# Kernel optimization log

Hardware: AMD Instinct MI355X
Metric: run time of the kernel (lower is better)

Reference implementation:

```python
import jax, jax.numpy as jnp
import numpy as np

DIM = 1024
MULT = 4
HID = DIM * MULT
E = 8
B, S = 2, 2048


def _rmsnorm(x):
    # zeta SimpleRMSNorm: F.normalize(x, dim=-1) * sqrt(dim)
    n = jnp.linalg.norm(x, axis=-1, keepdims=True)
    return x / jnp.maximum(n, 1e-12) * jnp.sqrt(jnp.asarray(x.shape[-1], x.dtype))


def _act_quant(x):
    # per-token 8-bit absmax quant (BitNet b1.58), straight-through in fwd math
    scale = 127.0 / jnp.clip(jnp.max(jnp.abs(x), axis=-1, keepdims=True), 1e-5)
    q = jnp.clip(jnp.round(x * scale), -128, 127) / scale
    return x + jax.lax.stop_gradient(q - x)


def _w_quant(w, axes):
    # ternary weight quant with per-matrix mean-abs scale
    scale = 1.0 / jnp.clip(jnp.mean(jnp.abs(w), axis=axes, keepdims=True), 1e-5)
    q = jnp.clip(jnp.round(w * scale), -1, 1) / scale
    return w + jax.lax.stop_gradient(q - w)


def setup_inputs() -> dict:
    key = jax.random.key(0)
    ks = jax.random.split(key, 8)
    sd = 0.02
    x = jax.random.normal(ks[0], (B, S, DIM), dtype=jnp.float32)
    gw = jax.random.normal(ks[1], (E, DIM), dtype=jnp.float32) * sd
    gb = jnp.zeros((E,), dtype=jnp.float32)
    w1 = jax.random.normal(ks[2], (E, HID, DIM), dtype=jnp.float32) * sd
    b1 = jnp.zeros((E, HID), dtype=jnp.float32)
    w2 = jax.random.normal(ks[3], (E, DIM, HID), dtype=jnp.float32) * sd
    b2 = jnp.zeros((E, DIM), dtype=jnp.float32)
    return {"x": x, "gw": gw, "gb": gb, "w1": w1, "b1": b1, "w2": w2, "b2": b2}


def reference(x, gw, gb, w1, b1, w2, b2):
    # BitLinear input preprocessing: RMSNorm then 8-bit activation quant
    xq = _act_quant(_rmsnorm(x))  # [B,S,D]

    # Gate: softmax(BitLinear(dim, E))
    logits = jnp.einsum("bsd,ed->bse", xq, _w_quant(gw, axes=(0, 1))) + gb
    gates = jax.nn.softmax(logits, axis=-1)  # [B,S,E]

    # Experts: BitLinear -> GELU -> BitLinear, quant scales per expert
    w1q = _w_quant(w1, axes=(1, 2))  # [E,H,D]
    w2q = _w_quant(w2, axes=(1, 2))  # [E,D,H]
    h = jnp.einsum("bsd,ehd->bseh", xq, w1q) + b1  # [B,S,E,H]
    a = jax.nn.gelu(h, approximate=False)
    aq = _act_quant(_rmsnorm(a))
    expert_out = jnp.einsum("bseh,edh->bsed", aq, w2q) + b2  # [B,S,E,D]

    # softmax-weighted sum over experts
    return jnp.einsum("bse,bsed->bsd", gates, expert_out)
```

## Files before the change

### kernel.cpp

```cpp
#include <hip/hip_runtime.h>


#define T_TOK 4096
#define DIMS  1024
#define HID   4096
#define NE    8
#define ROWB  8192ull

typedef __attribute__((ext_vector_type(4))) int       i32x4;
typedef __attribute__((ext_vector_type(8))) _Float16  f16x8;

__device__ __forceinline__ float block_sum(float v, float* buf, int tid) {
  #pragma unroll
  for (int o = 32; o > 0; o >>= 1) v += __shfl_down(v, o, 64);
  __syncthreads();
  if ((tid & 63) == 0) buf[tid >> 6] = v;
  __syncthreads();
  return buf[0] + buf[1] + buf[2] + buf[3];
}
__device__ __forceinline__ float block_max(float v, float* buf, int tid) {
  #pragma unroll
  for (int o = 32; o > 0; o >>= 1) { float t = __shfl_down(v, o, 64); v = fmaxf(v, t); }
  __syncthreads();
  if ((tid & 63) == 0) buf[tid >> 6] = v;
  __syncthreads();
  return fmaxf(fmaxf(buf[0], buf[1]), fmaxf(buf[2], buf[3]));
}

__device__ __forceinline__ void gl_lds16(const void* g, void* l) {
  __builtin_amdgcn_global_load_lds(
      (const __attribute__((address_space(1))) unsigned int*)g,
      (__attribute__((address_space(3))) unsigned int*)l, 16, 0, 0);
}

__device__ __forceinline__ int q8(float v) {
  return ((int)fminf(fmaxf(rintf(v), -128.0f), 127.0f)) & 0xff;
}

__device__ __forceinline__ const i32x4* frag(const char* s, int row, int ckW) {
  return (const i32x4*)&s[row * 128 + ((ckW ^ (row & 7)) << 4)];
}

__global__ __launch_bounds__(256) void wabs_sum_kernel(
    const float4* __restrict__ w, int n_f4, int shift, float* __restrict__ sums) {
  __shared__ float buf[4];
  const int tid = threadIdx.x;
  const int base = blockIdx.x * 4096;
  float acc = 0.0f;
  for (int k = 0; k < 16; ++k) {
    int fi = base + k * 256 + tid;
    if (fi < n_f4) {
      float4 v = w[fi];
      acc += fabsf(v.x) + fabsf(v.y) + fabsf(v.z) + fabsf(v.w);
    }
  }
  acc = block_sum(acc, buf, tid);
  if (tid == 0) atomicAdd(&sums[base >> shift], acc);
}

__global__ void mkscales_kernel(const float* __restrict__ wsum, float* __restrict__ sc) {
  if (threadIdx.x == 0) {
    #pragma unroll
    for (int e = 0; e < NE; ++e) {
      float m1 = fmaxf(wsum[e] * (1.0f / 4194304.0f), 1e-5f);
      sc[e] = m1; sc[8 + e] = 1.0f / m1;
      float m2 = fmaxf(wsum[8 + e] * (1.0f / 4194304.0f), 1e-5f);
      sc[16 + e] = m2; sc[24 + e] = 1.0f / m2;
    }
    float mg = fmaxf(wsum[16] * (1.0f / 8192.0f), 1e-5f);
    sc[32] = mg; sc[33] = 1.0f / mg;
  }
}

__global__ __launch_bounds__(256) void wquant_kernel(
    const float4* __restrict__ w, int* __restrict__ o, int n_f4, int shift,
    const float* __restrict__ qs) {
  int fi = blockIdx.x * 256 + threadIdx.x;
  if (fi >= n_f4) return;
  const float s = qs[fi >> shift];
  float4 v = w[fi];
  int b0 = ((int)fminf(fmaxf(rintf(v.x * s), -1.0f), 1.0f)) & 0xff;
  int b1 = ((int)fminf(fmaxf(rintf(v.y * s), -1.0f), 1.0f)) & 0xff;
  int b2 = ((int)fminf(fmaxf(rintf(v.z * s), -1.0f), 1.0f)) & 0xff;
  int b3 = ((int)fminf(fmaxf(rintf(v.w * s), -1.0f), 1.0f)) & 0xff;
  o[fi] = b0 | (b1 << 8) | (b2 << 16) | (b3 << 24);
}

__global__ __launch_bounds__(256) void preprocess_kernel(
    const float* __restrict__ x, const float* __restrict__ gw,
    const float* __restrict__ gb, const float* __restrict__ scales,
    int* __restrict__ qx, float* __restrict__ inv_sx, float* __restrict__ gates) {
  __shared__ float buf[4];
  const int t = blockIdx.x, tid = threadIdx.x;
  const float4 xv = ((const float4*)(x + (size_t)t * DIMS))[tid];
  float ss = xv.x * xv.x + xv.y * xv.y + xv.z * xv.z + xv.w * xv.w;
  ss = block_sum(ss, buf, tid);
  const float rr = 32.0f / fmaxf(sqrtf(ss), 1e-12f);
  const float y0 = xv.x * rr, y1 = xv.y * rr, y2 = xv.z * rr, y3 = xv.w * rr;
  float am = fmaxf(fmaxf(fabsf(y0), fabsf(y1)), fmaxf(fabsf(y2), fabsf(y3)));
  am = block_max(am, buf, tid);
  const float aclip = fmaxf(am, 1e-5f);
  const float qsc = 127.0f / aclip;
  const float q0 = fminf(fmaxf(rintf(y0 * qsc), -128.0f), 127.0f);
  const float q1 = fminf(fmaxf(rintf(y1 * qsc), -128.0f), 127.0f);
  const float q2 = fminf(fmaxf(rintf(y2 * qsc), -128.0f), 127.0f);
  const float q3 = fminf(fmaxf(rintf(y3 * qsc), -128.0f), 127.0f);
  qx[t * 256 + tid] = (((int)q0) & 0xff) | ((((int)q1) & 0xff) << 8) |
                      ((((int)q2) & 0xff) << 16) | ((((int)q3) & 0xff) << 24);

  const float gsabs = scales[32], gqs = scales[33];
  float lg[NE];
  #pragma unroll
  for (int e = 0; e < NE; ++e) {
    const float4 gv = ((const float4*)(gw + e * DIMS))[tid];
    float t0 = fminf(fmaxf(rintf(gv.x * gqs), -1.0f), 1.0f);
    float t1 = fminf(fmaxf(rintf(gv.y * gqs), -1.0f), 1.0f);
    float t2 = fminf(fmaxf(rintf(gv.z * gqs), -1.0f), 1.0f);
    float t3 = fminf(fmaxf(rintf(gv.w * gqs), -1.0f), 1.0f);
    lg[e] = q0 * t0 + q1 * t1 + q2 * t2 + q3 * t3;
  }
  #pragma unroll
  for (int e = 0; e < NE; ++e) lg[e] = block_sum(lg[e], buf, tid);
  if (tid == 0) {
    const float isx = aclip / 127.0f;
    inv_sx[t] = isx;
    float l[NE], mx = -1e30f;
    #pragma unroll
    for (int e = 0; e < NE; ++e) { l[e] = lg[e] * (isx * gsabs) + gb[e]; mx = fmaxf(mx, l[e]); }
    float s = 0.0f;
    #pragma unroll
    for (int e = 0; e < NE; ++e) { l[e] = expf(l[e] - mx); s += l[e]; }
    const float inv = 1.0f / s;
    #pragma unroll
    for (int e = 0; e < NE; ++e) gates[t * NE + e] = l[e] * inv;
  }
}

__global__ __launch_bounds__(256, 2) void gemm1_kernel(
    const char* __restrict__ qx, const char* __restrict__ w1q,
    const float* __restrict__ scales, const float* __restrict__ inv_sx,
    const float* __restrict__ b1, char* __restrict__ aqa) {
  __shared__ __align__(16) char sA[256 * 128];
  __shared__ __align__(16) char sB[128 * 128];
  const int e = blockIdx.z;
  const char* A = qx;
  const char* Bm = w1q + (size_t)e * HID * DIMS;
  char* obase = aqa + (size_t)e * T_TOK * ROWB;
  const int n0 = blockIdx.x * 128, m0 = blockIdx.y * 256;
  const int tid = threadIdx.x, lane = tid & 63, wv = tid >> 6;
  const int wr = (wv >> 1) * 128, wc = (wv & 1) * 64, lm = lane & 15, lq = lane >> 4;
  i32x4 acc[8][4] = {};
  for (int k0 = 0; k0 < DIMS; k0 += 128) {
    #pragma unroll
    for (int it = 0; it < 8; ++it) {
      const int c = it * 256 + tid;
      const int row = c >> 3, ckG = (c & 7) ^ (row & 7);
      gl_lds16(A + (size_t)(m0 + row) * DIMS + k0 + ckG * 16, &sA[c * 16]);
    }
    #pragma unroll
    for (int it = 0; it < 4; ++it) {
      const int c = it * 256 + tid;
      const int row = c >> 3, ckG = (c & 7) ^ (row & 7);
      gl_lds16(Bm + (size_t)(n0 + row) * DIMS + k0 + ckG * 16, &sB[c * 16]);
    }
    __syncthreads();
    #pragma unroll
    for (int kk = 0; kk < 2; ++kk) {
      i32x4 av[8], bv[4];
      const int ckW = kk * 4 + lq;
      #pragma unroll
      for (int i = 0; i < 8; ++i) av[i] = *frag(sA, wr + i * 16 + lm, ckW);
      #pragma unroll
      for (int j = 0; j < 4; ++j) bv[j] = *frag(sB, wc + j * 16 + lm, ckW);
      #pragma unroll
      for (int i = 0; i < 8; ++i)
        #pragma unroll
        for (int j = 0; j < 4; ++j)
          acc[i][j] = __builtin_amdgcn_mfma_i32_16x16x64_i8(av[i], bv[j], acc[i][j], 0, 0, 0);
    }
    __syncthreads();
  }
  const float s1 = scales[e];
  #pragma unroll
  for (int i = 0; i < 8; ++i) {
    #pragma unroll
    for (int r = 0; r < 4; ++r) {
      const int row = m0 + wr + i * 16 + lq * 4 + r;
      const float rs = inv_sx[row] * s1;
      _Float16* orow = (_Float16*)(obase + (size_t)row * ROWB);
      #pragma unroll
      for (int j = 0; j < 4; ++j) {
        const int col = n0 + wc + j * 16 + lm;
        const float h = (float)acc[i][j][r] * rs + b1[e * HID + col];
        const float a = 0.5f * h * (1.0f + erff(h * 0.70710678118654752f));
        orow[col] = (_Float16)a;
      }
    }
  }
}

__global__ __launch_bounds__(256) void rowquant_kernel(
    char* __restrict__ aqa, float* __restrict__ inv_sa) {
  __shared__ float buf[4];
  const size_t R = blockIdx.x;
  char* rowb = aqa + R * ROWB;
  const int tid = threadIdx.x;
  f16x8 v0 = ((const f16x8*)rowb)[tid * 2];
  f16x8 v1 = ((const f16x8*)rowb)[tid * 2 + 1];
  float f[16];
  #pragma unroll
  for (int k = 0; k < 8; ++k) { f[k] = (float)v0[k]; f[8 + k] = (float)v1[k]; }
  float ss = 0.0f;
  #pragma unroll
  for (int k = 0; k < 16; ++k) ss += f[k] * f[k];
  ss = block_sum(ss, buf, tid);
  const float rr = 64.0f / fmaxf(sqrtf(ss), 1e-12f);
  float am = 0.0f;
  #pragma unroll
  for (int k = 0; k < 16; ++k) am = fmaxf(am, fabsf(f[k] * rr));
  am = block_max(am, buf, tid);
  const float aclip = fmaxf(am, 1e-5f);
  const float qsc = rr * 127.0f / aclip;
  int4 o;
  o.x = q8(f[0] * qsc) | (q8(f[1] * qsc) << 8) | (q8(f[2] * qsc) << 16) | (q8(f[3] * qsc) << 24);
  o.y = q8(f[4] * qsc) | (q8(f[5] * qsc) << 8) | (q8(f[6] * qsc) << 16) | (q8(f[7] * qsc) << 24);
  o.z = q8(f[8] * qsc) | (q8(f[9] * qsc) << 8) | (q8(f[10] * qsc) << 16) | (q8(f[11] * qsc) << 24);
  o.w = q8(f[12] * qsc) | (q8(f[13] * qsc) << 8) | (q8(f[14] * qsc) << 16) | (q8(f[15] * qsc) << 24);
  ((int4*)rowb)[tid] = o;
  if (tid == 0) inv_sa[R] = aclip / 127.0f;
}

__global__ __launch_bounds__(256, 2) void gemm2_kernel(
    const char* __restrict__ aqa, const char* __restrict__ w2q,
    const float* __restrict__ scales, const float* __restrict__ inv_sa,
    const float* __restrict__ b2, const float* __restrict__ gates,
    float* __restrict__ dst, int use_atomic) {
  __shared__ __align__(16) char sA[256 * 128];
  __shared__ __align__(16) char sB[128 * 128];
  const int e = blockIdx.z;
  const char* A = aqa + (size_t)e * T_TOK * ROWB;
  const char* Bm = w2q + (size_t)e * DIMS * HID;
  const int n0 = blockIdx.x * 128, m0 = blockIdx.y * 256;
  const int tid = threadIdx.x, lane = tid & 63, wv = tid >> 6;
  const int wr = (wv >> 1) * 128, wc = (wv & 1) * 64, lm = lane & 15, lq = lane >> 4;
  i32x4 acc[8][4] = {};
  for (int k0 = 0; k0 < HID; k0 += 128) {
    #pragma unroll
    for (int it = 0; it < 8; ++it) {
      const int c = it * 256 + tid;
      const int row = c >> 3, ckG = (c & 7) ^ (row & 7);
      gl_lds16(A + (size_t)(m0 + row) * ROWB + k0 + ckG * 16, &sA[c * 16]);
    }
    #pragma unroll
    for (int it = 0; it < 4; ++it) {
      const int c = it * 256 + tid;
      const int row = c >> 3, ckG = (c & 7) ^ (row & 7);
      gl_lds16(Bm + (size_t)(n0 + row) * HID + k0 + ckG * 16, &sB[c * 16]);
    }
    __syncthreads();
    #pragma unroll
    for (int kk = 0; kk < 2; ++kk) {
      i32x4 av[8], bv[4];
      const int ckW = kk * 4 + lq;
      #pragma unroll
      for (int i = 0; i < 8; ++i) av[i] = *frag(sA, wr + i * 16 + lm, ckW);
      #pragma unroll
      for (int j = 0; j < 4; ++j) bv[j] = *frag(sB, wc + j * 16 + lm, ckW);
      #pragma unroll
      for (int i = 0; i < 8; ++i)
        #pragma unroll
        for (int j = 0; j < 4; ++j)
          acc[i][j] = __builtin_amdgcn_mfma_i32_16x16x64_i8(av[i], bv[j], acc[i][j], 0, 0, 0);
    }
    __syncthreads();
  }
  const float s2 = scales[16 + e];
  #pragma unroll
  for (int i = 0; i < 8; ++i) {
    #pragma unroll
    for (int r = 0; r < 4; ++r) {
      const int row = m0 + wr + i * 16 + lq * 4 + r;
      const float rs = inv_sa[(size_t)e * T_TOK + row] * s2;
      const float g = gates[row * NE + e];
      #pragma unroll
      for (int j = 0; j < 4; ++j) {
        const int col = n0 + wc + j * 16 + lm;
        const float v = g * ((float)acc[i][j][r] * rs + b2[e * DIMS + col]);
        if (use_atomic) atomicAdd(&dst[(size_t)row * DIMS + col], v);
        else dst[((size_t)e * T_TOK + row) * DIMS + col] = v;
      }
    }
  }
}

__global__ __launch_bounds__(256) void reduce_kernel(
    const float4* __restrict__ eout, float4* __restrict__ out) {
  const int i = blockIdx.x * 256 + threadIdx.x;
  float4 s = eout[i];
  #pragma unroll
  for (int e = 1; e < NE; ++e) {
    float4 v = eout[(size_t)e * (T_TOK * DIMS / 4) + i];
    s.x += v.x; s.y += v.y; s.z += v.z; s.w += v.w;
  }
  out[i] = s;
}

extern "C" void kernel_launch(void* const* d_in, const int* in_sizes, int n_in,
                              void* d_out, int out_size, void* d_ws, size_t ws_size,
                              hipStream_t stream) {
  const float* x  = (const float*)d_in[0];
  const float* gw = (const float*)d_in[1];
  const float* gb = (const float*)d_in[2];
  const float* w1 = (const float*)d_in[3];
  const float* b1 = (const float*)d_in[4];
  const float* w2 = (const float*)d_in[5];
  const float* b2 = (const float*)d_in[6];
  float* outp = (float*)d_out;
  char* ws = (char*)d_ws;

  float* wsum   = (float*)(ws + 0);
  float* scales = (float*)(ws + 256);
  float* inv_sx = (float*)(ws + 4096);
  float* gates  = (float*)(ws + 20480);
  float* inv_sa = (float*)(ws + 151552);
  char*  qx     = ws + 282624;
  char*  w1q    = ws + 4476928;
  char*  w2q    = ws + 38031360;
  char*  aqa    = ws + 71585792;
  float* eout   = (float*)(ws + 340021248);

  const bool has_eout = ws_size >= 474238976ull;

  hipMemsetAsync(wsum, 0, 17 * sizeof(float), stream);
  wabs_sum_kernel<<<2048, 256, 0, stream>>>((const float4*)w1, 8388608, 20, wsum + 0);
  wabs_sum_kernel<<<2048, 256, 0, stream>>>((const float4*)w2, 8388608, 20, wsum + 8);
  wabs_sum_kernel<<<1,    256, 0, stream>>>((const float4*)gw, 2048,    30, wsum + 16);
  mkscales_kernel<<<1, 64, 0, stream>>>(wsum, scales);
  wquant_kernel<<<32768, 256, 0, stream>>>((const float4*)w1, (int*)w1q, 8388608, 20, scales + 8);
  wquant_kernel<<<32768, 256, 0, stream>>>((const float4*)w2, (int*)w2q, 8388608, 20, scales + 24);
  preprocess_kernel<<<4096, 256, 0, stream>>>(x, gw, gb, scales, (int*)qx, inv_sx, gates);

  gemm1_kernel<<<dim3(32, 16, 8), 256, 0, stream>>>(qx, w1q, scales, inv_sx, b1, aqa);
  rowquant_kernel<<<32768, 256, 0, stream>>>(aqa, inv_sa);

  if (has_eout) {
    gemm2_kernel<<<dim3(8, 16, 8), 256, 0, stream>>>(
        aqa, w2q, scales, inv_sa, b2, gates, eout, 0);
    reduce_kernel<<<4096, 256, 0, stream>>>((const float4*)eout, (float4*)outp);
  } else {
    hipMemsetAsync(outp, 0, (size_t)out_size * sizeof(float), stream);
    gemm2_kernel<<<dim3(8, 16, 8), 256, 0, stream>>>(
        aqa, w2q, scales, inv_sa, b2, gates, outp, 1);
  }
}
```

Baseline: 939.5 us.

## Move GELU into rowquant with fast erf, store expert outputs as fp16

The gemm1 epilogue now stores the pre-activation value as fp16, and GELU is applied in the rowquant kernel using a polynomial erf approximation built on rcp and exp. The gemm2 non-atomic path writes gated per-expert outputs as fp16 instead of fp32, which halves the intermediate buffer traffic and the reduce kernel's reads. Bias loads are hoisted out of the epilogue loops. This trades some accuracy for less work: the erf approximation error is around 1e-7, the pre-activation is rounded to fp16 before GELU, and the expert partial sums are rounded to fp16 before the fp32 reduction.

Result: faster. 891.9 us (-5.1%).

```diff
diff --git a/kernel.cpp b/kernel.cpp
--- a/kernel.cpp
+++ b/kernel.cpp
@@ -35,6 +35,22 @@
 
 __device__ __forceinline__ int q8(float v) {
   return ((int)fminf(fmaxf(rintf(v), -128.0f), 127.0f)) & 0xff;
+}
+
+__device__ __forceinline__ float erf_fast(float x) {
+  const float ax = fabsf(x);
+  const float t = __builtin_amdgcn_rcpf(fmaf(0.3275911f, ax, 1.0f));
+  float p = fmaf(1.061405429f, t, -1.453152027f);
+  p = fmaf(p, t, 1.421413741f);
+  p = fmaf(p, t, -0.284496736f);
+  p = fmaf(p, t, 0.254829592f);
+  p = p * t;
+  const float e = __expf(-ax * ax);
+  const float r = fmaf(-p, e, 1.0f);
+  return copysignf(r, x);
+}
+__device__ __forceinline__ float gelu_fast(float h) {
+  return 0.5f * h * (1.0f + erf_fast(h * 0.70710678118654752f));
 }
 
 __device__ __forceinline__ const i32x4* frag(const char* s, int row, int ckW) {
@@ -181,6 +197,9 @@
     __syncthreads();
   }
   const float s1 = scales[e];
+  float bb[4];
+  #pragma unroll
+  for (int j = 0; j < 4; ++j) bb[j] = b1[e * HID + n0 + wc + j * 16 + lm];
   #pragma unroll
   for (int i = 0; i < 8; ++i) {
     #pragma unroll
@@ -191,9 +210,7 @@
       #pragma unroll
       for (int j = 0; j < 4; ++j) {
         const int col = n0 + wc + j * 16 + lm;
-        const float h = (float)acc[i][j][r] * rs + b1[e * HID + col];
-        const float a = 0.5f * h * (1.0f + erff(h * 0.70710678118654752f));
-        orow[col] = (_Float16)a;
+        orow[col] = (_Float16)fmaf((float)acc[i][j][r], rs, bb[j]);
       }
     }
   }
@@ -210,6 +227,8 @@
   float f[16];
   #pragma unroll
   for (int k = 0; k < 8; ++k) { f[k] = (float)v0[k]; f[8 + k] = (float)v1[k]; }
+  #pragma unroll
+  for (int k = 0; k < 16; ++k) f[k] = gelu_fast(f[k]);
   float ss = 0.0f;
   #pragma unroll
   for (int k = 0; k < 16; ++k) ss += f[k] * f[k];
@@ -234,7 +253,7 @@
     const char* __restrict__ aqa, const char* __restrict__ w2q,
     const float* __restrict__ scales, const float* __restrict__ inv_sa,
     const float* __restrict__ b2, const float* __restrict__ gates,
-    float* __restrict__ dst, int use_atomic) {
+    void* __restrict__ dstv, int use_atomic) {
   __shared__ __align__(16) char sA[256 * 128];
   __shared__ __align__(16) char sB[128 * 128];
   const int e = blockIdx.z;
@@ -275,6 +294,9 @@
     __syncthreads();
   }
   const float s2 = scales[16 + e];
+  float bb[4];
+  #pragma unroll
+  for (int j = 0; j < 4; ++j) bb[j] = b2[e * DIMS + n0 + wc + j * 16 + lm];
   #pragma unroll
   for (int i = 0; i < 8; ++i) {
     #pragma unroll
@@ -285,24 +307,28 @@
       #pragma unroll
       for (int j = 0; j < 4; ++j) {
         const int col = n0 + wc + j * 16 + lm;
-        const float v = g * ((float)acc[i][j][r] * rs + b2[e * DIMS + col]);
-        if (use_atomic) atomicAdd(&dst[(size_t)row * DIMS + col], v);
-        else dst[((size_t)e * T_TOK + row) * DIMS + col] = v;
+        const float v = g * fmaf((float)acc[i][j][r], rs, bb[j]);
+        if (use_atomic) atomicAdd(&((float*)dstv)[(size_t)row * DIMS + col], v);
+        else ((_Float16*)dstv)[((size_t)e * T_TOK + row) * DIMS + col] = (_Float16)v;
       }
     }
   }
 }
 
 __global__ __launch_bounds__(256) void reduce_kernel(
-    const float4* __restrict__ eout, float4* __restrict__ out) {
+    const f16x8* __restrict__ eout, float4* __restrict__ out) {
   const int i = blockIdx.x * 256 + threadIdx.x;
-  float4 s = eout[i];
-  #pragma unroll
-  for (int e = 1; e < NE; ++e) {
-    float4 v = eout[(size_t)e * (T_TOK * DIMS / 4) + i];
-    s.x += v.x; s.y += v.y; s.z += v.z; s.w += v.w;
-  }
-  out[i] = s;
+  float s[8] = {};
+  #pragma unroll
+  for (int e = 0; e < NE; ++e) {
+    f16x8 v = eout[(size_t)e * (T_TOK * DIMS / 8) + i];
+    #pragma unroll
+    for (int k = 0; k < 8; ++k) s[k] += (float)v[k];
+  }
+  float4 o0; o0.x = s[0]; o0.y = s[1]; o0.z = s[2]; o0.w = s[3];
+  float4 o1; o1.x = s[4]; o1.y = s[5]; o1.z = s[6]; o1.w = s[7];
+  out[i * 2]     = o0;
+  out[i * 2 + 1] = o1;
 }
 
 extern "C" void kernel_launch(void* const* d_in, const int* in_sizes, int n_in,
@@ -327,9 +353,9 @@
   char*  w1q    = ws + 4476928;
   char*  w2q    = ws + 38031360;
   char*  aqa    = ws + 71585792;
-  float* eout   = (float*)(ws + 340021248);
-
-  const bool has_eout = ws_size >= 474238976ull;
+  char*  eout   = ws + 340021248;
+
+  const bool has_eout = ws_size >= 340021248ull + 67108864ull;
 
   hipMemsetAsync(wsum, 0, 17 * sizeof(float), stream);
   wabs_sum_kernel<<<2048, 256, 0, stream>>>((const float4*)w1, 8388608, 20, wsum + 0);
@@ -346,7 +372,7 @@
   if (has_eout) {
     gemm2_kernel<<<dim3(8, 16, 8), 256, 0, stream>>>(
         aqa, w2q, scales, inv_sa, b2, gates, eout, 0);
-    reduce_kernel<<<4096, 256, 0, stream>>>((const float4*)eout, (float4*)outp);
+    reduce_kernel<<<2048, 256, 0, stream>>>((const f16x8*)eout, (float4*)outp);
   } else {
     hipMemsetAsync(outp, 0, (size_t)out_size * sizeof(float), stream);
     gemm2_kernel<<<dim3(8, 16, 8), 256, 0, stream>>>(
```
